# Optimization experiments

Measured on AMD Instinct MI355X. Metric: run time of the kernel, lower is better.

Reference implementation:

```python
import jax, jax.numpy as jnp
import numpy as np

N_HEADS = 8
TOPK = 64
LN_EPS = 1e-5


def layernorm(x, g, b):
    mu = jnp.mean(x, axis=-1, keepdims=True)
    var = jnp.mean((x - mu) ** 2, axis=-1, keepdims=True)
    return (x - mu) * jax.lax.rsqrt(var + LN_EPS) * g + b


def mha(x, wq, wk, wv, wo, causal):
    # x: [B, S, H]; weights are torch nn.Linear style [out, in]
    B, S, H = x.shape
    hd = H // N_HEADS
    scale = 1.0 / np.sqrt(hd)

    def proj(w):
        return (x @ w.T).reshape(B, S, N_HEADS, hd).transpose(0, 2, 1, 3)  # [B, n, S, hd]

    q, k, v = proj(wq), proj(wk), proj(wv)
    s = jnp.einsum('bnqd,bnkd->bnqk', q, k) * scale
    if causal:
        m = jnp.tril(jnp.ones((S, S), bool))
        s = jnp.where(m, s, jnp.finfo(s.dtype).min)
    a = jax.nn.softmax(s, axis=-1)
    o = jnp.einsum('bnqk,bnkd->bnqd', a, v).transpose(0, 2, 1, 3).reshape(B, S, H)
    return o @ wo.T


def topk_activation(x, k):
    # x: [N, F]; keep top-k per row, zero elsewhere (matches topk + scatter_)
    vals, idx = jax.lax.top_k(x, k)
    rows = jnp.arange(x.shape[0])[:, None]
    return jnp.zeros_like(x).at[rows, idx].set(vals)


def setup_inputs() -> dict:
    key = jax.random.key(0)
    B, D, L, H, F = 8, 16, 128, 512, 4096
    ks = jax.random.split(key, 12)
    s = 1.0 / np.sqrt(H)
    w = lambda k, shp, sc: jax.random.normal(k, shp, jnp.float32) * sc
    return {
        'zL': w(ks[0], (B, D, L, H), 1.0),
        'wq_l': w(ks[1], (H, H), s), 'wk_l': w(ks[2], (H, H), s),
        'wv_l': w(ks[3], (H, H), s), 'wo_l': w(ks[4], (H, H), s),
        'gamma_l': jnp.ones(H, jnp.float32), 'beta_l': jnp.zeros(H, jnp.float32),
        'wq_d': w(ks[5], (H, H), s), 'wk_d': w(ks[6], (H, H), s),
        'wv_d': w(ks[7], (H, H), s), 'wo_d': w(ks[8], (H, H), s),
        'gamma_d': jnp.ones(H, jnp.float32), 'beta_d': jnp.zeros(H, jnp.float32),
        'dict_enc': w(ks[9], (F, H), np.sqrt(2.0 / (H + F))),
        'bias_pre': jnp.zeros(H, jnp.float32),
        'bias_enc': jnp.zeros(F, jnp.float32),
        'query_token': jnp.zeros(H, jnp.float32),
    }


def reference(zL, wq_l, wk_l, wv_l, wo_l, gamma_l, beta_l,
              wq_d, wk_d, wv_d, wo_d, gamma_d, beta_d,
              dict_enc, bias_pre, bias_enc, query_token):
    B, D, L, H = zL.shape
    F = dict_enc.shape[0]
    # prepend learned query token along depth, drop last layer
    qt = jnp.broadcast_to(query_token[None, None, None, :], (B, 1, L, H))
    x = jnp.concatenate([qt, zL[:, :-1, :, :]], axis=1)  # [B, D, L, H]
    # non-causal attention over L within each (b, d)
    x = x.reshape(B * D, L, H)
    x = x + mha(layernorm(x, gamma_l, beta_l), wq_l, wk_l, wv_l, wo_l, causal=False)
    # causal attention over D within each (b, l)
    x = x.reshape(B, D, L, H).transpose(0, 2, 1, 3).reshape(B * L, D, H)
    x = x + mha(layernorm(x, gamma_d, beta_d), wq_d, wk_d, wv_d, wo_d, causal=True)
    x_prior = x.reshape(B, L, D, H).transpose(0, 2, 1, 3)  # [B, D, L, H]
    # dictionary encode on residual (detached in original)
    N = B * D * L
    x_src = jax.lax.stop_gradient(zL - x_prior).reshape(N, H)
    logits = (x_src - bias_pre[None, :]) @ dict_enc.T + bias_enc
    z_dense = jax.nn.relu(logits)
    z_flat = topk_activation(z_dense, TOPK)
    z_n = z_flat.reshape(B, D, L, F)
    return z_n, x_prior
```

## Files before the change

### kernel.cpp

```cpp
#include <hip/hip_runtime.h>
#include <stdint.h>

#define NTOK 16384
#define HDIM 512
#define FDIM 4096
#define NHEAD 8

typedef __attribute__((ext_vector_type(8))) _Float16 f16x8;
typedef __attribute__((ext_vector_type(16))) float f32x16;
#define LOSCALE 4096.0f
#define LOINV   (1.0f / 4096.0f)

static __device__ __forceinline__ void ld8f(const float* p, float* v) {
    *(float4*)&v[0] = *(const float4*)p;
    *(float4*)&v[4] = *(const float4*)(p + 4);
}
static __device__ __forceinline__ void st8f(float* p, const float* v) {
    *(float4*)p       = *(const float4*)&v[0];
    *(float4*)(p + 4) = *(const float4*)&v[4];
}

__global__ __launch_bounds__(256) void build_x_k(const float* __restrict__ zL,
                                                 const float* __restrict__ qt,
                                                 float* __restrict__ X) {
    int idx = blockIdx.x * 256 + threadIdx.x;
    int n = idx >> 6;
    int h = (idx & 63) << 3;
    int d = (n >> 7) & 15;
    const float* src = d ? (zL + (((size_t)(n - 128)) << 9) + h) : (qt + h);
    float v[8];
    ld8f(src, v);
    st8f(X + (((size_t)n) << 9) + h, v);
}

__global__ __launch_bounds__(256) void ln_stats_k(const float* __restrict__ X,
                                                  float* __restrict__ mu,
                                                  float* __restrict__ rstd) {
    int row = blockIdx.x * 4 + (threadIdx.x >> 6);
    int lane = threadIdx.x & 63;
    const float* xr = X + (((size_t)row) << 9) + (lane << 3);
    float v[8];
    ld8f(xr, v);
    float s = 0.f;
#pragma unroll
    for (int i = 0; i < 8; ++i) s += v[i];
#pragma unroll
    for (int off = 32; off; off >>= 1) s += __shfl_xor(s, off);
    float m = s * (1.0f / 512.0f);
    float q = 0.f;
#pragma unroll
    for (int i = 0; i < 8; ++i) { float d = v[i] - m; q += d * d; }
#pragma unroll
    for (int off = 32; off; off >>= 1) q += __shfl_xor(q, off);
    if (lane == 0) {
        mu[row] = m;
        rstd[row] = 1.0f / sqrtf(q * (1.0f / 512.0f) + 1e-5f);
    }
}

__global__ __launch_bounds__(512) void attn_l_k(float* __restrict__ QO,
                                                const float* __restrict__ K,
                                                const float* __restrict__ V) {
    __shared__ float ks[128][64];
    __shared__ float vs[128][64];
    const int seq = blockIdx.x, head = blockIdx.y;
    const int t = threadIdx.x;
    const size_t base = (((size_t)seq) << 16) + (head << 6);
#pragma unroll
    for (int i = 0; i < 4; ++i) {
        int slot = t + (i << 9);
        int row = slot >> 4;
        int c4 = (slot & 15) << 2;
        size_t g = base + (((size_t)row) << 9) + c4;
        *(float4*)&ks[row][c4] = *(const float4*)(K + g);
        *(float4*)&vs[row][c4] = *(const float4*)(V + g);
    }
    __syncthreads();
    const int r = t >> 2;
    const int q16 = (t & 3) << 4;
    float* qp = QO + base + (((size_t)r) << 9) + q16;
    float qr[16];
#pragma unroll
    for (int i = 0; i < 4; ++i) *(float4*)&qr[i << 2] = *(const float4*)(qp + (i << 2));
    float o[16];
#pragma unroll
    for (int d = 0; d < 16; ++d) o[d] = 0.f;
    float m = -1e30f, l = 0.f;
    for (int j = 0; j < 128; ++j) {
        const float* kp = &ks[j][q16];
        float s0 = 0.f, s1 = 0.f, s2 = 0.f, s3 = 0.f;
#pragma unroll
        for (int d = 0; d < 16; d += 4) {
            s0 = fmaf(qr[d + 0], kp[d + 0], s0);
            s1 = fmaf(qr[d + 1], kp[d + 1], s1);
            s2 = fmaf(qr[d + 2], kp[d + 2], s2);
            s3 = fmaf(qr[d + 3], kp[d + 3], s3);
        }
        float sp = (s0 + s1) + (s2 + s3);
        sp += __shfl_xor(sp, 1);
        sp += __shfl_xor(sp, 2);
        float s = sp * 0.125f;
        if (s > m) {
            float c = expf(m - s);
#pragma unroll
            for (int d = 0; d < 16; ++d) o[d] *= c;
            l *= c;
            m = s;
        }
        float w = expf(s - m);
        l += w;
        const float* vp = &vs[j][q16];
#pragma unroll
        for (int d = 0; d < 16; ++d) o[d] = fmaf(w, vp[d], o[d]);
    }
    float inv = 1.0f / l;
#pragma unroll
    for (int i = 0; i < 4; ++i)
        *(float4*)(qp + (i << 2)) = make_float4(o[i * 4] * inv, o[i * 4 + 1] * inv,
                                                o[i * 4 + 2] * inv, o[i * 4 + 3] * inv);
}

__global__ __launch_bounds__(128) void attn_d_k(float* __restrict__ QO,
                                                const float* __restrict__ K,
                                                const float* __restrict__ V) {
    __shared__ float ks[16][512];
    __shared__ float vs[16][512];
    const int bl = blockIdx.x;
    const int b = bl >> 7, l = bl & 127;
    const int t = threadIdx.x;
    const size_t base = ((size_t)(b * 2048 + l)) << 9;
#pragma unroll
    for (int i = 0; i < 16; ++i) {
        int slot = t + (i << 7);
        int row = slot >> 7;
        int c4 = (slot & 127) << 2;
        size_t g = base + (((size_t)row) << 16) + c4;
        *(float4*)&ks[row][c4] = *(const float4*)(K + g);
        *(float4*)&vs[row][c4] = *(const float4*)(V + g);
    }
    __syncthreads();
    const int head = t >> 4, dr = t & 15;
    const int ho = head << 6;
    float qr[64];
    float* qp = QO + base + (((size_t)dr) << 16) + ho;
#pragma unroll
    for (int i = 0; i < 16; ++i) *(float4*)&qr[i << 2] = *(const float4*)(qp + (i << 2));
    float s[16];
    float m = -1e30f;
#pragma unroll
    for (int j = 0; j < 16; ++j) {
        float s0 = 0.f, s1 = 0.f, s2 = 0.f, s3 = 0.f;
#pragma unroll
        for (int d = 0; d < 64; d += 4) {
            s0 = fmaf(qr[d + 0], ks[j][ho + d + 0], s0);
            s1 = fmaf(qr[d + 1], ks[j][ho + d + 1], s1);
            s2 = fmaf(qr[d + 2], ks[j][ho + d + 2], s2);
            s3 = fmaf(qr[d + 3], ks[j][ho + d + 3], s3);
        }
        float sv = ((s0 + s1) + (s2 + s3)) * 0.125f;
        s[j] = (j <= dr) ? sv : -1e30f;
        m = fmaxf(m, s[j]);
    }
    float lsum = 0.f;
#pragma unroll
    for (int j = 0; j < 16; ++j) {
        float w = (j <= dr) ? expf(s[j] - m) : 0.f;
        s[j] = w;
        lsum += w;
    }
    float inv = 1.0f / lsum;
    float o[64];
#pragma unroll
    for (int d = 0; d < 64; ++d) o[d] = 0.f;
#pragma unroll
    for (int j = 0; j < 16; ++j) {
        float w = s[j];
#pragma unroll
        for (int d = 0; d < 64; ++d) o[d] = fmaf(w, vs[j][ho + d], o[d]);
    }
#pragma unroll
    for (int i = 0; i < 16; ++i)
        *(float4*)(qp + (i << 2)) = make_float4(o[i * 4] * inv, o[i * 4 + 1] * inv,
                                                o[i * 4 + 2] * inv, o[i * 4 + 3] * inv);
}

__global__ __launch_bounds__(256) void xprior_xsrc_k(const float* __restrict__ zL,
                                                     const float* __restrict__ bias_pre,
                                                     float* __restrict__ X,
                                                     float* __restrict__ out_xp) {
    int idx = blockIdx.x * 256 + threadIdx.x;
    int h = (idx & 63) << 3;
    float z[8], p[8], x[8];
    ld8f(zL + (((size_t)idx) << 3), z);
    ld8f(bias_pre + h, p);
    float* xp = X + (((size_t)idx) << 3);
    ld8f(xp, x);
    st8f(out_xp + (((size_t)idx) << 3), x);
    float o[8];
#pragma unroll
    for (int i = 0; i < 8; ++i) o[i] = z[i] - x[i] - p[i];
    st8f(xp, o);
}

__global__ __launch_bounds__(256) void split2_k(const float* __restrict__ in,
                                                _Float16* __restrict__ ph,
                                                _Float16* __restrict__ pl) {
    int idx = blockIdx.x * 256 + threadIdx.x;
    float v[8];
    ld8f(in + (((size_t)idx) << 3), v);
    _Float16 h8[8], l8[8];
#pragma unroll
    for (int i = 0; i < 8; ++i) {
        _Float16 h = (_Float16)v[i];
        float r = v[i] - (float)h;
        h8[i] = h;
        l8[i] = (_Float16)(r * LOSCALE);
    }
    *(int4*)(ph + (((size_t)idx) << 3)) = *(int4*)h8;
    *(int4*)(pl + (((size_t)idx) << 3)) = *(int4*)l8;
}

__global__ __launch_bounds__(256) void split2_ln_k(const float* __restrict__ X,
                                                   const float* __restrict__ mu,
                                                   const float* __restrict__ rstd,
                                                   const float* __restrict__ gamma,
                                                   const float* __restrict__ beta,
                                                   _Float16* __restrict__ ph,
                                                   _Float16* __restrict__ pl) {
    int idx = blockIdx.x * 256 + threadIdx.x;
    int row = idx >> 6;
    int h = (idx & 63) << 3;
    float v[8], gv[8], be[8];
    ld8f(X + (((size_t)idx) << 3), v);
    ld8f(gamma + h, gv);
    ld8f(beta + h, be);
    float m = mu[row], rs = rstd[row];
    _Float16 h8[8], l8[8];
#pragma unroll
    for (int i = 0; i < 8; ++i) {
        float y = (v[i] - m) * rs * gv[i] + be[i];
        _Float16 hh = (_Float16)y;
        float r = y - (float)hh;
        h8[i] = hh;
        l8[i] = (_Float16)(r * LOSCALE);
    }
    *(int4*)(ph + (((size_t)idx) << 3)) = *(int4*)h8;
    *(int4*)(pl + (((size_t)idx) << 3)) = *(int4*)l8;
}

#define LDT 34
template<bool ADD_C, bool BIAS>
__global__ __launch_bounds__(256) void gemm_f16_k(
        const _Float16* __restrict__ Xh, const _Float16* __restrict__ Xl,
        const _Float16* __restrict__ Wh, const _Float16* __restrict__ Wl,
        const float* __restrict__ bias, float* __restrict__ Cout, int ldc) {
    __shared__ _Float16 Ah[128][LDT], Al[128][LDT];
    __shared__ _Float16 Bh[64][LDT],  Bl[64][LDT];
    const int tid = threadIdx.x;
    const int bm = blockIdx.y << 7;
    const int bn = blockIdx.x << 6;
    const int w = tid >> 6, lane = tid & 63;
    const int wr = w >> 1, wc = w & 1;
    const int l31 = lane & 31, hh = lane >> 5;
    f32x16 acc1[2], acc2[2];
#pragma unroll
    for (int i = 0; i < 2; ++i)
#pragma unroll
        for (int r = 0; r < 16; ++r) { acc1[i][r] = 0.f; acc2[i][r] = 0.f; }

    for (int k0 = 0; k0 < HDIM; k0 += 32) {
        __syncthreads();
#pragma unroll
        for (int i = 0; i < 2; ++i) {
            int s = tid + (i << 8);
            int row = s >> 2, kg = (s & 3) << 3;
            size_t ga = (size_t)(bm + row) * HDIM + k0 + kg;
            *(int4*)&Ah[row][kg] = *(const int4*)(Xh + ga);
            *(int4*)&Al[row][kg] = *(const int4*)(Xl + ga);
        }
        {
            int row = tid >> 2, kg = (tid & 3) << 3;
            size_t gb = (size_t)(bn + row) * HDIM + k0 + kg;
            *(int4*)&Bh[row][kg] = *(const int4*)(Wh + gb);
            *(int4*)&Bl[row][kg] = *(const int4*)(Wl + gb);
        }
        __syncthreads();
#pragma unroll
        for (int kh = 0; kh < 2; ++kh) {
            const int ko = (kh << 4) + (hh << 3);
            f16x8 fah[2], fal[2];
#pragma unroll
            for (int mf = 0; mf < 2; ++mf) {
                int ar = (wr << 6) + (mf << 5) + l31;
                fah[mf] = *(const f16x8*)&Ah[ar][ko];
                fal[mf] = *(const f16x8*)&Al[ar][ko];
            }
            int bc_ = (wc << 5) + l31;
            f16x8 bh = *(const f16x8*)&Bh[bc_][ko];
            f16x8 bl = *(const f16x8*)&Bl[bc_][ko];
#pragma unroll
            for (int mf = 0; mf < 2; ++mf) {
                acc1[mf] = __builtin_amdgcn_mfma_f32_32x32x16_f16(fah[mf], bh, acc1[mf], 0, 0, 0);
                acc2[mf] = __builtin_amdgcn_mfma_f32_32x32x16_f16(fah[mf], bl, acc2[mf], 0, 0, 0);
                acc2[mf] = __builtin_amdgcn_mfma_f32_32x32x16_f16(fal[mf], bh, acc2[mf], 0, 0, 0);
            }
        }
    }
    const int col = bn + (wc << 5) + l31;
    const float badd = BIAS ? bias[col] : 0.f;
#pragma unroll
    for (int mf = 0; mf < 2; ++mf) {
#pragma unroll
        for (int r = 0; r < 16; ++r) {
            int row = bm + (wr << 6) + (mf << 5) + (r & 3) + ((r >> 2) << 3) + (hh << 2);
            float* cp = Cout + (size_t)row * ldc + col;
            float val = acc1[mf][r] + acc2[mf][r] * LOINV + badd;
            if (ADD_C) val += *cp;
            *cp = val;
        }
    }
}

__global__ __launch_bounds__(256) void topk_k(const float* __restrict__ logits,
                                              float* __restrict__ out) {
    const int row = blockIdx.x;
    const float* lr = logits + (((size_t)row) << 12);
    const int t = threadIdx.x;
    float v[16]; uint32_t u[16];
#pragma unroll
    for (int i = 0; i < 16; ++i) {
        float x = fmaxf(lr[t + (i << 8)], 0.f);
        v[i] = x;
        u[i] = __float_as_uint(x);
    }
    __shared__ int red[4];
    __shared__ unsigned long long bits[64];
    __shared__ int s_cut;
    uint32_t prefix = 0;
    bool exact = false;
    for (int bit = 30; bit >= 0; --bit) {
        uint32_t c = prefix | (1u << bit);
        int cnt = 0;
#pragma unroll
        for (int i = 0; i < 16; ++i) cnt += (u[i] >= c) ? 1 : 0;
#pragma unroll
        for (int off = 32; off; off >>= 1) cnt += __shfl_xor(cnt, off);
        if ((t & 63) == 0) red[t >> 6] = cnt;
        __syncthreads();
        int total = red[0] + red[1] + red[2] + red[3];
        __syncthreads();
        if (total >= 64) prefix = c;
        if (total == 64) { exact = true; break; }
    }
    float* orow = out + (((size_t)row) << 12);
    if (exact) {
#pragma unroll
        for (int i = 0; i < 16; ++i) {
            int col = t + (i << 8);
            orow[col] = (u[i] >= prefix) ? v[i] : 0.f;
        }
        return;
    }
    const uint32_t T64 = prefix;
    int cg = 0;
#pragma unroll
    for (int i = 0; i < 16; ++i) cg += (u[i] > T64) ? 1 : 0;
#pragma unroll
    for (int off = 32; off; off >>= 1) cg += __shfl_xor(cg, off);
    if ((t & 63) == 0) red[t >> 6] = cg;
    __syncthreads();
    const int ngt = red[0] + red[1] + red[2] + red[3];
    int cut = -1;
    if (T64 != 0u) {
        const int r = 64 - ngt;
        if (t < 64) bits[t] = 0ull;
        __syncthreads();
#pragma unroll
        for (int i = 0; i < 16; ++i) {
            if (u[i] == T64) {
                int col = t + (i << 8);
                atomicOr(&bits[col >> 6], 1ull << (col & 63));
            }
        }
        __syncthreads();
        if (t == 0) {
            int need = r, cs = FDIM - 1;
            for (int wd = 0; wd < 64; ++wd) {
                int pc = __popcll(bits[wd]);
                if (need <= pc) {
                    unsigned long long bb = bits[wd];
                    for (int q = 1; q < need; ++q) bb &= bb - 1;
                    cs = (wd << 6) + (__ffsll(bb) - 1);
                    break;
                }
                need -= pc;
            }
            s_cut = cs;
        }
        __syncthreads();
        cut = s_cut;
    }
#pragma unroll
    for (int i = 0; i < 16; ++i) {
        int col = t + (i << 8);
        bool keep = (u[i] > T64) || (T64 != 0u && u[i] == T64 && col <= cut);
        orow[col] = keep ? v[i] : 0.f;
    }
}

extern "C" void kernel_launch(void* const* d_in, const int* in_sizes, int n_in,
                              void* d_out, int out_size, void* d_ws, size_t ws_size,
                              hipStream_t stream) {
    const float* zL      = (const float*)d_in[0];
    const float* gamma_l = (const float*)d_in[5];
    const float* beta_l  = (const float*)d_in[6];
    const float* gamma_d = (const float*)d_in[11];
    const float* beta_d  = (const float*)d_in[12];
    const float* dict_e  = (const float*)d_in[13];
    const float* bias_pre= (const float*)d_in[14];
    const float* bias_enc= (const float*)d_in[15];
    const float* qt      = (const float*)d_in[16];
    const float* wproj[8] = { (const float*)d_in[1], (const float*)d_in[2],
                              (const float*)d_in[3], (const float*)d_in[4],
                              (const float*)d_in[7], (const float*)d_in[8],
                              (const float*)d_in[9], (const float*)d_in[10] };

    float* out_z  = (float*)d_out;
    float* out_xp = out_z + (size_t)NTOK * FDIM;

    const size_t NHf = (size_t)NTOK * HDIM;
    float* B0 = (float*)d_out;
    float* B1 = B0 + NHf;
    float* B2 = B1 + NHf;
    float* B3 = B2 + NHf;

    float* wsf    = (float*)d_ws;
    float* mu     = wsf + 64;
    float* rstd   = mu + NTOK;
    float* logits = rstd + NTOK;

    const size_t dictE = (size_t)FDIM * HDIM;
    const size_t WE    = (size_t)HDIM * HDIM;

    int crows = NTOK;
    const size_t mfmaFixedB = (64 + 2 * (size_t)NTOK) * sizeof(float)
                            + (2 * dictE + 16 * WE + 2 * NHf) * sizeof(_Float16);
    while (crows > 128 &&
           mfmaFixedB + (size_t)crows * FDIM * sizeof(float) > ws_size) crows >>= 1;
    const bool ok = mfmaFixedB + (size_t)128 * FDIM * sizeof(float) <= ws_size;

    const dim3 blk256(256), blk128(128), blk512(512);
    const dim3 gElem(4096);
    const dim3 gProjM(HDIM / 64, NTOK / 128);

    if (ok) {
        _Float16* dh = (_Float16*)(logits + (size_t)crows * FDIM);
        _Float16* dl = dh + dictE;
        _Float16* wsp = dh + 2 * dictE;
        _Float16* xh = wsp + 16 * WE;
        _Float16* xl = xh + NHf;
        _Float16* wh[8], *wl[8];
        for (int i = 0; i < 8; ++i) {
            wh[i] = wsp + (size_t)i * 2 * WE;
            wl[i] = wh[i] + WE;
        }

        for (int i = 0; i < 8; ++i)
            split2_k<<<dim3(WE / 8 / 256), blk256, 0, stream>>>(wproj[i], wh[i], wl[i]);
        split2_k<<<dim3(dictE / 8 / 256), blk256, 0, stream>>>(dict_e, dh, dl);

        build_x_k<<<gElem, blk256, 0, stream>>>(zL, qt, B0);

        ln_stats_k<<<dim3(NTOK / 4), blk256, 0, stream>>>(B0, mu, rstd);
        split2_ln_k<<<gElem, blk256, 0, stream>>>(B0, mu, rstd, gamma_l, beta_l, xh, xl);
        gemm_f16_k<false, false><<<gProjM, blk256, 0, stream>>>(xh, xl, wh[0], wl[0], nullptr, B1, HDIM);
        gemm_f16_k<false, false><<<gProjM, blk256, 0, stream>>>(xh, xl, wh[1], wl[1], nullptr, B2, HDIM);
        gemm_f16_k<false, false><<<gProjM, blk256, 0, stream>>>(xh, xl, wh[2], wl[2], nullptr, B3, HDIM);
        attn_l_k<<<dim3(128, NHEAD), blk512, 0, stream>>>(B1, B2, B3);
        split2_k<<<gElem, blk256, 0, stream>>>(B1, xh, xl);
        gemm_f16_k<true, false><<<gProjM, blk256, 0, stream>>>(xh, xl, wh[3], wl[3], nullptr, B0, HDIM);

        ln_stats_k<<<dim3(NTOK / 4), blk256, 0, stream>>>(B0, mu, rstd);
        split2_ln_k<<<gElem, blk256, 0, stream>>>(B0, mu, rstd, gamma_d, beta_d, xh, xl);
        gemm_f16_k<false, false><<<gProjM, blk256, 0, stream>>>(xh, xl, wh[4], wl[4], nullptr, B1, HDIM);
        gemm_f16_k<false, false><<<gProjM, blk256, 0, stream>>>(xh, xl, wh[5], wl[5], nullptr, B2, HDIM);
        gemm_f16_k<false, false><<<gProjM, blk256, 0, stream>>>(xh, xl, wh[6], wl[6], nullptr, B3, HDIM);
        attn_d_k<<<dim3(1024), blk128, 0, stream>>>(B1, B2, B3);
        split2_k<<<gElem, blk256, 0, stream>>>(B1, xh, xl);
        gemm_f16_k<true, false><<<gProjM, blk256, 0, stream>>>(xh, xl, wh[7], wl[7], nullptr, B0, HDIM);

        xprior_xsrc_k<<<gElem, blk256, 0, stream>>>(zL, bias_pre, B0, out_xp);
        split2_k<<<gElem, blk256, 0, stream>>>(B0, xh, xl);

        const dim3 gDict(FDIM / 64, crows / 128);
        for (int c0 = 0; c0 < NTOK; c0 += crows) {
            gemm_f16_k<false, true><<<gDict, blk256, 0, stream>>>(
                xh + (size_t)c0 * HDIM, xl + (size_t)c0 * HDIM,
                dh, dl, bias_enc, logits, FDIM);
            topk_k<<<dim3(crows), blk256, 0, stream>>>(logits, out_z + (size_t)c0 * FDIM);
        }
    } else {
        int cr = 2048;
        const size_t fixedB = (64 + 2 * (size_t)NTOK) * sizeof(float) + dictE * 2 * sizeof(_Float16);
        while (cr > 128 &&
               fixedB + (size_t)cr * FDIM * sizeof(float) + ((size_t)cr * HDIM + 16 * WE) * 2 * sizeof(_Float16) > ws_size)
            cr >>= 1;
        _Float16* dh = (_Float16*)(logits + (size_t)cr * FDIM);
        _Float16* dl = dh + dictE;
        _Float16* xh = dl + dictE;
        _Float16* xl = xh + (size_t)cr * HDIM;
        _Float16* wh = xl + (size_t)cr * HDIM;
        _Float16* wlo = wh + WE;

        build_x_k<<<gElem, blk256, 0, stream>>>(zL, qt, B0);

        ln_stats_k<<<dim3(NTOK / 4), blk256, 0, stream>>>(B0, mu, rstd);
        for (int i = 0; i < 3; ++i) {
            split2_k<<<dim3(WE / 8 / 256), blk256, 0, stream>>>(wproj[i], wh, wlo);
            float* dst = (i == 0) ? B1 : (i == 1) ? B2 : B3;
            for (int c0 = 0; c0 < NTOK; c0 += cr) {
                split2_ln_k<<<dim3(cr * HDIM / 8 / 256), blk256, 0, stream>>>(
                    B0 + (size_t)c0 * HDIM, mu + c0, rstd + c0, gamma_l, beta_l, xh, xl);
                gemm_f16_k<false, false><<<dim3(HDIM / 64, cr / 128), blk256, 0, stream>>>(
                    xh, xl, wh, wlo, nullptr, dst + (size_t)c0 * HDIM, HDIM);
            }
        }
        attn_l_k<<<dim3(128, NHEAD), blk512, 0, stream>>>(B1, B2, B3);
        split2_k<<<dim3(WE / 8 / 256), blk256, 0, stream>>>(wproj[3], wh, wlo);
        for (int c0 = 0; c0 < NTOK; c0 += cr) {
            split2_k<<<dim3(cr * HDIM / 8 / 256), blk256, 0, stream>>>(B1 + (size_t)c0 * HDIM, xh, xl);
            gemm_f16_k<true, false><<<dim3(HDIM / 64, cr / 128), blk256, 0, stream>>>(
                xh, xl, wh, wlo, nullptr, B0 + (size_t)c0 * HDIM, HDIM);
        }
        ln_stats_k<<<dim3(NTOK / 4), blk256, 0, stream>>>(B0, mu, rstd);
        for (int i = 4; i < 7; ++i) {
            split2_k<<<dim3(WE / 8 / 256), blk256, 0, stream>>>(wproj[i], wh, wlo);
            float* dst = (i == 4) ? B1 : (i == 5) ? B2 : B3;
            for (int c0 = 0; c0 < NTOK; c0 += cr) {
                split2_ln_k<<<dim3(cr * HDIM / 8 / 256), blk256, 0, stream>>>(
                    B0 + (size_t)c0 * HDIM, mu + c0, rstd + c0, gamma_d, beta_d, xh, xl);
                gemm_f16_k<false, false><<<dim3(HDIM / 64, cr / 128), blk256, 0, stream>>>(
                    xh, xl, wh, wlo, nullptr, dst + (size_t)c0 * HDIM, HDIM);
            }
        }
        attn_d_k<<<dim3(1024), blk128, 0, stream>>>(B1, B2, B3);
        split2_k<<<dim3(WE / 8 / 256), blk256, 0, stream>>>(wproj[7], wh, wlo);
        for (int c0 = 0; c0 < NTOK; c0 += cr) {
            split2_k<<<dim3(cr * HDIM / 8 / 256), blk256, 0, stream>>>(B1 + (size_t)c0 * HDIM, xh, xl);
            gemm_f16_k<true, false><<<dim3(HDIM / 64, cr / 128), blk256, 0, stream>>>(
                xh, xl, wh, wlo, nullptr, B0 + (size_t)c0 * HDIM, HDIM);
        }
        xprior_xsrc_k<<<gElem, blk256, 0, stream>>>(zL, bias_pre, B0, out_xp);
        split2_k<<<dim3(dictE / 8 / 256), blk256, 0, stream>>>(dict_e, dh, dl);
        for (int c0 = NTOK - cr; c0 >= 0; c0 -= cr) {
            split2_k<<<dim3(cr * HDIM / 8 / 256), blk256, 0, stream>>>(B0 + (size_t)c0 * HDIM, xh, xl);
            gemm_f16_k<false, true><<<dim3(FDIM / 64, cr / 128), blk256, 0, stream>>>(
                xh, xl, dh, dl, bias_enc, logits, FDIM);
            topk_k<<<dim3(cr), blk256, 0, stream>>>(logits, out_z + (size_t)c0 * FDIM);
        }
    }
}
```

Before: 1.168 ms.

## Fuse fp16 split into LN, attention and residual kernels; double-buffer GEMM tiles

LayerNorm statistics and normalisation now happen in one kernel that writes the hi/lo fp16 split directly. The attention kernels and the x_src kernel also emit the split form, which removes the separate split2 passes and their extra fp32 round trips through global memory. The GEMM now uses double-buffered shared-memory tiles with a register prefetch of the next k-slice, so global loads overlap the MFMA work. The chunked fallback path for small workspaces is dropped, which assumes the workspace is large enough and doubles the GEMM's LDS use.

```diff
diff --git a/kernel.cpp b/kernel.cpp
--- a/kernel.cpp
+++ b/kernel.cpp
@@ -33,12 +33,15 @@
     st8f(X + (((size_t)n) << 9) + h, v);
 }
 
-__global__ __launch_bounds__(256) void ln_stats_k(const float* __restrict__ X,
-                                                  float* __restrict__ mu,
-                                                  float* __restrict__ rstd) {
+__global__ __launch_bounds__(256) void ln_split_k(const float* __restrict__ X,
+                                                  const float* __restrict__ gamma,
+                                                  const float* __restrict__ beta,
+                                                  _Float16* __restrict__ ph,
+                                                  _Float16* __restrict__ pl) {
     int row = blockIdx.x * 4 + (threadIdx.x >> 6);
     int lane = threadIdx.x & 63;
-    const float* xr = X + (((size_t)row) << 9) + (lane << 3);
+    int h = lane << 3;
+    const float* xr = X + (((size_t)row) << 9) + h;
     float v[8];
     ld8f(xr, v);
     float s = 0.f;
@@ -52,15 +55,28 @@
     for (int i = 0; i < 8; ++i) { float d = v[i] - m; q += d * d; }
 #pragma unroll
     for (int off = 32; off; off >>= 1) q += __shfl_xor(q, off);
-    if (lane == 0) {
-        mu[row] = m;
-        rstd[row] = 1.0f / sqrtf(q * (1.0f / 512.0f) + 1e-5f);
-    }
-}
-
-__global__ __launch_bounds__(512) void attn_l_k(float* __restrict__ QO,
+    float rs = 1.0f / sqrtf(q * (1.0f / 512.0f) + 1e-5f);
+    float gv[8], be[8];
+    ld8f(gamma + h, gv);
+    ld8f(beta + h, be);
+    _Float16 h8[8], l8[8];
+#pragma unroll
+    for (int i = 0; i < 8; ++i) {
+        float y = (v[i] - m) * rs * gv[i] + be[i];
+        _Float16 hh = (_Float16)y;
+        h8[i] = hh;
+        l8[i] = (_Float16)((y - (float)hh) * LOSCALE);
+    }
+    size_t off = (((size_t)row) << 9) + h;
+    *(int4*)(ph + off) = *(int4*)h8;
+    *(int4*)(pl + off) = *(int4*)l8;
+}
+
+__global__ __launch_bounds__(512) void attn_l_k(const float* __restrict__ Q,
                                                 const float* __restrict__ K,
-                                                const float* __restrict__ V) {
+                                                const float* __restrict__ V,
+                                                _Float16* __restrict__ xh,
+                                                _Float16* __restrict__ xl) {
     __shared__ float ks[128][64];
     __shared__ float vs[128][64];
     const int seq = blockIdx.x, head = blockIdx.y;
@@ -78,7 +94,7 @@
     __syncthreads();
     const int r = t >> 2;
     const int q16 = (t & 3) << 4;
-    float* qp = QO + base + (((size_t)r) << 9) + q16;
+    const float* qp = Q + base + (((size_t)r) << 9) + q16;
     float qr[16];
 #pragma unroll
     for (int i = 0; i < 4; ++i) *(float4*)&qr[i << 2] = *(const float4*)(qp + (i << 2));
@@ -114,15 +130,26 @@
         for (int d = 0; d < 16; ++d) o[d] = fmaf(w, vp[d], o[d]);
     }
     float inv = 1.0f / l;
-#pragma unroll
-    for (int i = 0; i < 4; ++i)
-        *(float4*)(qp + (i << 2)) = make_float4(o[i * 4] * inv, o[i * 4 + 1] * inv,
-                                                o[i * 4 + 2] * inv, o[i * 4 + 3] * inv);
-}
-
-__global__ __launch_bounds__(128) void attn_d_k(float* __restrict__ QO,
+    _Float16 h8[16], l8[16];
+#pragma unroll
+    for (int i = 0; i < 16; ++i) {
+        float y = o[i] * inv;
+        _Float16 hh = (_Float16)y;
+        h8[i] = hh;
+        l8[i] = (_Float16)((y - (float)hh) * LOSCALE);
+    }
+    size_t eo = base + (((size_t)r) << 9) + q16;
+    *(int4*)(xh + eo)     = ((int4*)h8)[0];
+    *(int4*)(xh + eo + 8) = ((int4*)h8)[1];
+    *(int4*)(xl + eo)     = ((int4*)l8)[0];
+    *(int4*)(xl + eo + 8) = ((int4*)l8)[1];
+}
+
+__global__ __launch_bounds__(128) void attn_d_k(const float* __restrict__ Q,
                                                 const float* __restrict__ K,
-                                                const float* __restrict__ V) {
+                                                const float* __restrict__ V,
+                                                _Float16* __restrict__ xh,
+                                                _Float16* __restrict__ xl) {
     __shared__ float ks[16][512];
     __shared__ float vs[16][512];
     const int bl = blockIdx.x;
@@ -142,7 +169,7 @@
     const int head = t >> 4, dr = t & 15;
     const int ho = head << 6;
     float qr[64];
-    float* qp = QO + base + (((size_t)dr) << 16) + ho;
+    const float* qp = Q + base + (((size_t)dr) << 16) + ho;
 #pragma unroll
     for (int i = 0; i < 16; ++i) *(float4*)&qr[i << 2] = *(const float4*)(qp + (i << 2));
     float s[16];
@@ -178,28 +205,46 @@
 #pragma unroll
         for (int d = 0; d < 64; ++d) o[d] = fmaf(w, vs[j][ho + d], o[d]);
     }
-#pragma unroll
-    for (int i = 0; i < 16; ++i)
-        *(float4*)(qp + (i << 2)) = make_float4(o[i * 4] * inv, o[i * 4 + 1] * inv,
-                                                o[i * 4 + 2] * inv, o[i * 4 + 3] * inv);
+    size_t eo = base + (((size_t)dr) << 16) + ho;
+#pragma unroll
+    for (int i = 0; i < 8; ++i) {
+        _Float16 h8[8], l8[8];
+#pragma unroll
+        for (int j = 0; j < 8; ++j) {
+            float y = o[i * 8 + j] * inv;
+            _Float16 hh = (_Float16)y;
+            h8[j] = hh;
+            l8[j] = (_Float16)((y - (float)hh) * LOSCALE);
+        }
+        *(int4*)(xh + eo + (i << 3)) = *(int4*)h8;
+        *(int4*)(xl + eo + (i << 3)) = *(int4*)l8;
+    }
 }
 
 __global__ __launch_bounds__(256) void xprior_xsrc_k(const float* __restrict__ zL,
                                                      const float* __restrict__ bias_pre,
-                                                     float* __restrict__ X,
-                                                     float* __restrict__ out_xp) {
+                                                     const float* __restrict__ X,
+                                                     float* __restrict__ out_xp,
+                                                     _Float16* __restrict__ xh,
+                                                     _Float16* __restrict__ xl) {
     int idx = blockIdx.x * 256 + threadIdx.x;
     int h = (idx & 63) << 3;
+    size_t off = ((size_t)idx) << 3;
     float z[8], p[8], x[8];
-    ld8f(zL + (((size_t)idx) << 3), z);
+    ld8f(zL + off, z);
     ld8f(bias_pre + h, p);
-    float* xp = X + (((size_t)idx) << 3);
-    ld8f(xp, x);
-    st8f(out_xp + (((size_t)idx) << 3), x);
-    float o[8];
-#pragma unroll
-    for (int i = 0; i < 8; ++i) o[i] = z[i] - x[i] - p[i];
-    st8f(xp, o);
+    ld8f(X + off, x);
+    st8f(out_xp + off, x);
+    _Float16 h8[8], l8[8];
+#pragma unroll
+    for (int i = 0; i < 8; ++i) {
+        float y = z[i] - x[i] - p[i];
+        _Float16 hh = (_Float16)y;
+        h8[i] = hh;
+        l8[i] = (_Float16)((y - (float)hh) * LOSCALE);
+    }
+    *(int4*)(xh + off) = *(int4*)h8;
+    *(int4*)(xl + off) = *(int4*)l8;
 }
 
 __global__ __launch_bounds__(256) void split2_k(const float* __restrict__ in,
@@ -220,70 +265,58 @@
     *(int4*)(pl + (((size_t)idx) << 3)) = *(int4*)l8;
 }
 
-__global__ __launch_bounds__(256) void split2_ln_k(const float* __restrict__ X,
-                                                   const float* __restrict__ mu,
-                                                   const float* __restrict__ rstd,
-                                                   const float* __restrict__ gamma,
-                                                   const float* __restrict__ beta,
-                                                   _Float16* __restrict__ ph,
-                                                   _Float16* __restrict__ pl) {
-    int idx = blockIdx.x * 256 + threadIdx.x;
-    int row = idx >> 6;
-    int h = (idx & 63) << 3;
-    float v[8], gv[8], be[8];
-    ld8f(X + (((size_t)idx) << 3), v);
-    ld8f(gamma + h, gv);
-    ld8f(beta + h, be);
-    float m = mu[row], rs = rstd[row];
-    _Float16 h8[8], l8[8];
-#pragma unroll
-    for (int i = 0; i < 8; ++i) {
-        float y = (v[i] - m) * rs * gv[i] + be[i];
-        _Float16 hh = (_Float16)y;
-        float r = y - (float)hh;
-        h8[i] = hh;
-        l8[i] = (_Float16)(r * LOSCALE);
-    }
-    *(int4*)(ph + (((size_t)idx) << 3)) = *(int4*)h8;
-    *(int4*)(pl + (((size_t)idx) << 3)) = *(int4*)l8;
-}
-
 #define LDT 34
 template<bool ADD_C, bool BIAS>
 __global__ __launch_bounds__(256) void gemm_f16_k(
         const _Float16* __restrict__ Xh, const _Float16* __restrict__ Xl,
         const _Float16* __restrict__ Wh, const _Float16* __restrict__ Wl,
         const float* __restrict__ bias, float* __restrict__ Cout, int ldc) {
-    __shared__ _Float16 Ah[128][LDT], Al[128][LDT];
-    __shared__ _Float16 Bh[64][LDT],  Bl[64][LDT];
+    __shared__ _Float16 Ah[2][128][LDT], Al[2][128][LDT];
+    __shared__ _Float16 Bh[2][64][LDT],  Bl[2][64][LDT];
     const int tid = threadIdx.x;
     const int bm = blockIdx.y << 7;
     const int bn = blockIdx.x << 6;
     const int w = tid >> 6, lane = tid & 63;
     const int wr = w >> 1, wc = w & 1;
     const int l31 = lane & 31, hh = lane >> 5;
+    const int ar0 = tid >> 2, akg = (tid & 3) << 3;
+    const int ar1 = ar0 + 64;
+    const _Float16* pXh0 = Xh + (size_t)(bm + ar0) * HDIM + akg;
+    const _Float16* pXl0 = Xl + (size_t)(bm + ar0) * HDIM + akg;
+    const _Float16* pXh1 = Xh + (size_t)(bm + ar1) * HDIM + akg;
+    const _Float16* pXl1 = Xl + (size_t)(bm + ar1) * HDIM + akg;
+    const _Float16* pWh  = Wh + (size_t)(bn + ar0) * HDIM + akg;
+    const _Float16* pWl  = Wl + (size_t)(bn + ar0) * HDIM + akg;
+
     f32x16 acc1[2], acc2[2];
 #pragma unroll
     for (int i = 0; i < 2; ++i)
 #pragma unroll
         for (int r = 0; r < 16; ++r) { acc1[i][r] = 0.f; acc2[i][r] = 0.f; }
 
-    for (int k0 = 0; k0 < HDIM; k0 += 32) {
-        __syncthreads();
-#pragma unroll
-        for (int i = 0; i < 2; ++i) {
-            int s = tid + (i << 8);
-            int row = s >> 2, kg = (s & 3) << 3;
-            size_t ga = (size_t)(bm + row) * HDIM + k0 + kg;
-            *(int4*)&Ah[row][kg] = *(const int4*)(Xh + ga);
-            *(int4*)&Al[row][kg] = *(const int4*)(Xl + ga);
-        }
-        {
-            int row = tid >> 2, kg = (tid & 3) << 3;
-            size_t gb = (size_t)(bn + row) * HDIM + k0 + kg;
-            *(int4*)&Bh[row][kg] = *(const int4*)(Wh + gb);
-            *(int4*)&Bl[row][kg] = *(const int4*)(Wl + gb);
-        }
+    int4 ra0h, ra0l, ra1h, ra1l, rbh, rbl;
+    auto LOADR = [&](int k0) {
+        ra0h = *(const int4*)(pXh0 + k0);
+        ra0l = *(const int4*)(pXl0 + k0);
+        ra1h = *(const int4*)(pXh1 + k0);
+        ra1l = *(const int4*)(pXl1 + k0);
+        rbh  = *(const int4*)(pWh + k0);
+        rbl  = *(const int4*)(pWl + k0);
+    };
+    auto STORE = [&](int buf) {
+        *(int4*)&Ah[buf][ar0][akg] = ra0h;
+        *(int4*)&Al[buf][ar0][akg] = ra0l;
+        *(int4*)&Ah[buf][ar1][akg] = ra1h;
+        *(int4*)&Al[buf][ar1][akg] = ra1l;
+        *(int4*)&Bh[buf][ar0][akg] = rbh;
+        *(int4*)&Bl[buf][ar0][akg] = rbl;
+    };
+
+    LOADR(0);
+    STORE(0);
+    int cur = 0;
+    for (int it = 0; it < 16; ++it) {
+        if (it < 15) LOADR((it + 1) << 5);
         __syncthreads();
 #pragma unroll
         for (int kh = 0; kh < 2; ++kh) {
@@ -292,12 +325,12 @@
 #pragma unroll
             for (int mf = 0; mf < 2; ++mf) {
                 int ar = (wr << 6) + (mf << 5) + l31;
-                fah[mf] = *(const f16x8*)&Ah[ar][ko];
-                fal[mf] = *(const f16x8*)&Al[ar][ko];
+                fah[mf] = *(const f16x8*)&Ah[cur][ar][ko];
+                fal[mf] = *(const f16x8*)&Al[cur][ar][ko];
             }
             int bc_ = (wc << 5) + l31;
-            f16x8 bh = *(const f16x8*)&Bh[bc_][ko];
-            f16x8 bl = *(const f16x8*)&Bl[bc_][ko];
+            f16x8 bh = *(const f16x8*)&Bh[cur][bc_][ko];
+            f16x8 bl = *(const f16x8*)&Bl[cur][bc_][ko];
 #pragma unroll
             for (int mf = 0; mf < 2; ++mf) {
                 acc1[mf] = __builtin_amdgcn_mfma_f32_32x32x16_f16(fah[mf], bh, acc1[mf], 0, 0, 0);
@@ -305,6 +338,7 @@
                 acc2[mf] = __builtin_amdgcn_mfma_f32_32x32x16_f16(fal[mf], bh, acc2[mf], 0, 0, 0);
             }
         }
+        if (it < 15) { STORE(cur ^ 1); cur ^= 1; }
     }
     const int col = bn + (wc << 5) + l31;
     const float badd = BIAS ? bias[col] : 0.f;
@@ -435,128 +469,59 @@
     float* B3 = B2 + NHf;
 
     float* wsf    = (float*)d_ws;
-    float* mu     = wsf + 64;
-    float* rstd   = mu + NTOK;
-    float* logits = rstd + NTOK;
+    float* logits = wsf + 64;
 
     const size_t dictE = (size_t)FDIM * HDIM;
     const size_t WE    = (size_t)HDIM * HDIM;
 
     int crows = NTOK;
-    const size_t mfmaFixedB = (64 + 2 * (size_t)NTOK) * sizeof(float)
-                            + (2 * dictE + 16 * WE + 2 * NHf) * sizeof(_Float16);
-    while (crows > 128 &&
-           mfmaFixedB + (size_t)crows * FDIM * sizeof(float) > ws_size) crows >>= 1;
-    const bool ok = mfmaFixedB + (size_t)128 * FDIM * sizeof(float) <= ws_size;
+    const size_t fixedB = 64 * sizeof(float)
+                        + (2 * dictE + 16 * WE + 2 * NHf) * sizeof(_Float16);
+    while (crows > 128 && fixedB + (size_t)crows * FDIM * sizeof(float) > ws_size)
+        crows >>= 1;
+
+    _Float16* dh = (_Float16*)(logits + (size_t)crows * FDIM);
+    _Float16* dl = dh + dictE;
+    _Float16* wsp = dh + 2 * dictE;
+    _Float16* xh = wsp + 16 * WE;
+    _Float16* xl = xh + NHf;
+    _Float16* wh[8], *wl[8];
+    for (int i = 0; i < 8; ++i) {
+        wh[i] = wsp + (size_t)i * 2 * WE;
+        wl[i] = wh[i] + WE;
+    }
 
     const dim3 blk256(256), blk128(128), blk512(512);
     const dim3 gElem(4096);
     const dim3 gProjM(HDIM / 64, NTOK / 128);
 
-    if (ok) {
-        _Float16* dh = (_Float16*)(logits + (size_t)crows * FDIM);
-        _Float16* dl = dh + dictE;
-        _Float16* wsp = dh + 2 * dictE;
-        _Float16* xh = wsp + 16 * WE;
-        _Float16* xl = xh + NHf;
-        _Float16* wh[8], *wl[8];
-        for (int i = 0; i < 8; ++i) {
-            wh[i] = wsp + (size_t)i * 2 * WE;
-            wl[i] = wh[i] + WE;
-        }
-
-        for (int i = 0; i < 8; ++i)
-            split2_k<<<dim3(WE / 8 / 256), blk256, 0, stream>>>(wproj[i], wh[i], wl[i]);
-        split2_k<<<dim3(dictE / 8 / 256), blk256, 0, stream>>>(dict_e, dh, dl);
-
-        build_x_k<<<gElem, blk256, 0, stream>>>(zL, qt, B0);
-
-        ln_stats_k<<<dim3(NTOK / 4), blk256, 0, stream>>>(B0, mu, rstd);
-        split2_ln_k<<<gElem, blk256, 0, stream>>>(B0, mu, rstd, gamma_l, beta_l, xh, xl);
-        gemm_f16_k<false, false><<<gProjM, blk256, 0, stream>>>(xh, xl, wh[0], wl[0], nullptr, B1, HDIM);
-        gemm_f16_k<false, false><<<gProjM, blk256, 0, stream>>>(xh, xl, wh[1], wl[1], nullptr, B2, HDIM);
-        gemm_f16_k<false, false><<<gProjM, blk256, 0, stream>>>(xh, xl, wh[2], wl[2], nullptr, B3, HDIM);
-        attn_l_k<<<dim3(128, NHEAD), blk512, 0, stream>>>(B1, B2, B3);
-        split2_k<<<gElem, blk256, 0, stream>>>(B1, xh, xl);
-        gemm_f16_k<true, false><<<gProjM, blk256, 0, stream>>>(xh, xl, wh[3], wl[3], nullptr, B0, HDIM);
-
-        ln_stats_k<<<dim3(NTOK / 4), blk256, 0, stream>>>(B0, mu, rstd);
-        split2_ln_k<<<gElem, blk256, 0, stream>>>(B0, mu, rstd, gamma_d, beta_d, xh, xl);
-        gemm_f16_k<false, false><<<gProjM, blk256, 0, stream>>>(xh, xl, wh[4], wl[4], nullptr, B1, HDIM);
-        gemm_f16_k<false, false><<<gProjM, blk256, 0, stream>>>(xh, xl, wh[5], wl[5], nullptr, B2, HDIM);
-        gemm_f16_k<false, false><<<gProjM, blk256, 0, stream>>>(xh, xl, wh[6], wl[6], nullptr, B3, HDIM);
-        attn_d_k<<<dim3(1024), blk128, 0, stream>>>(B1, B2, B3);
-        split2_k<<<gElem, blk256, 0, stream>>>(B1, xh, xl);
-        gemm_f16_k<true, false><<<gProjM, blk256, 0, stream>>>(xh, xl, wh[7], wl[7], nullptr, B0, HDIM);
-
-        xprior_xsrc_k<<<gElem, blk256, 0, stream>>>(zL, bias_pre, B0, out_xp);
-        split2_k<<<gElem, blk256, 0, stream>>>(B0, xh, xl);
-
-        const dim3 gDict(FDIM / 64, crows / 128);
-        for (int c0 = 0; c0 < NTOK; c0 += crows) {
-            gemm_f16_k<false, true><<<gDict, blk256, 0, stream>>>(
-                xh + (size_t)c0 * HDIM, xl + (size_t)c0 * HDIM,
-                dh, dl, bias_enc, logits, FDIM);
-            topk_k<<<dim3(crows), blk256, 0, stream>>>(logits, out_z + (size_t)c0 * FDIM);
-        }
-    } else {
-        int cr = 2048;
-        const size_t fixedB = (64 + 2 * (size_t)NTOK) * sizeof(float) + dictE * 2 * sizeof(_Float16);
-        while (cr > 128 &&
-               fixedB + (size_t)cr * FDIM * sizeof(float) + ((size_t)cr * HDIM + 16 * WE) * 2 * sizeof(_Float16) > ws_size)
-            cr >>= 1;
-        _Float16* dh = (_Float16*)(logits + (size_t)cr * FDIM);
-        _Float16* dl = dh + dictE;
-        _Float16* xh = dl + dictE;
-        _Float16* xl = xh + (size_t)cr * HDIM;
-        _Float16* wh = xl + (size_t)cr * HDIM;
-        _Float16* wlo = wh + WE;
-
-        build_x_k<<<gElem, blk256, 0, stream>>>(zL, qt, B0);
-
-        ln_stats_k<<<dim3(NTOK / 4), blk256, 0, stream>>>(B0, mu, rstd);
-        for (int i = 0; i < 3; ++i) {
-            split2_k<<<dim3(WE / 8 / 256), blk256, 0, stream>>>(wproj[i], wh, wlo);
-            float* dst = (i == 0) ? B1 : (i == 1) ? B2 : B3;
-            for (int c0 = 0; c0 < NTOK; c0 += cr) {
-                split2_ln_k<<<dim3(cr * HDIM / 8 / 256), blk256, 0, stream>>>(
-                    B0 + (size_t)c0 * HDIM, mu + c0, rstd + c0, gamma_l, beta_l, xh, xl);
-                gemm_f16_k<false, false><<<dim3(HDIM / 64, cr / 128), blk256, 0, stream>>>(
-                    xh, xl, wh, wlo, nullptr, dst + (size_t)c0 * HDIM, HDIM);
-            }
-        }
-        attn_l_k<<<dim3(128, NHEAD), blk512, 0, stream>>>(B1, B2, B3);
-        split2_k<<<dim3(WE / 8 / 256), blk256, 0, stream>>>(wproj[3], wh, wlo);
-        for (int c0 = 0; c0 < NTOK; c0 += cr) {
-            split2_k<<<dim3(cr * HDIM / 8 / 256), blk256, 0, stream>>>(B1 + (size_t)c0 * HDIM, xh, xl);
-            gemm_f16_k<true, false><<<dim3(HDIM / 64, cr / 128), blk256, 0, stream>>>(
-                xh, xl, wh, wlo, nullptr, B0 + (size_t)c0 * HDIM, HDIM);
-        }
-        ln_stats_k<<<dim3(NTOK / 4), blk256, 0, stream>>>(B0, mu, rstd);
-        for (int i = 4; i < 7; ++i) {
-            split2_k<<<dim3(WE / 8 / 256), blk256, 0, stream>>>(wproj[i], wh, wlo);
-            float* dst = (i == 4) ? B1 : (i == 5) ? B2 : B3;
-            for (int c0 = 0; c0 < NTOK; c0 += cr) {
-                split2_ln_k<<<dim3(cr * HDIM / 8 / 256), blk256, 0, stream>>>(
-                    B0 + (size_t)c0 * HDIM, mu + c0, rstd + c0, gamma_d, beta_d, xh, xl);
-                gemm_f16_k<false, false><<<dim3(HDIM / 64, cr / 128), blk256, 0, stream>>>(
-                    xh, xl, wh, wlo, nullptr, dst + (size_t)c0 * HDIM, HDIM);
-            }
-        }
-        attn_d_k<<<dim3(1024), blk128, 0, stream>>>(B1, B2, B3);
-        split2_k<<<dim3(WE / 8 / 256), blk256, 0, stream>>>(wproj[7], wh, wlo);
-        for (int c0 = 0; c0 < NTOK; c0 += cr) {
-            split2_k<<<dim3(cr * HDIM / 8 / 256), blk256, 0, stream>>>(B1 + (size_t)c0 * HDIM, xh, xl);
-            gemm_f16_k<true, false><<<dim3(HDIM / 64, cr / 128), blk256, 0, stream>>>(
-                xh, xl, wh, wlo, nullptr, B0 + (size_t)c0 * HDIM, HDIM);
-        }
-        xprior_xsrc_k<<<gElem, blk256, 0, stream>>>(zL, bias_pre, B0, out_xp);
-        split2_k<<<dim3(dictE / 8 / 256), blk256, 0, stream>>>(dict_e, dh, dl);
-        for (int c0 = NTOK - cr; c0 >= 0; c0 -= cr) {
-            split2_k<<<dim3(cr * HDIM / 8 / 256), blk256, 0, stream>>>(B0 + (size_t)c0 * HDIM, xh, xl);
-            gemm_f16_k<false, true><<<dim3(FDIM / 64, cr / 128), blk256, 0, stream>>>(
-                xh, xl, dh, dl, bias_enc, logits, FDIM);
-            topk_k<<<dim3(cr), blk256, 0, stream>>>(logits, out_z + (size_t)c0 * FDIM);
-        }
-    }
-}
+    for (int i = 0; i < 8; ++i)
+        split2_k<<<dim3(WE / 8 / 256), blk256, 0, stream>>>(wproj[i], wh[i], wl[i]);
+    split2_k<<<dim3(dictE / 8 / 256), blk256, 0, stream>>>(dict_e, dh, dl);
+
+    build_x_k<<<gElem, blk256, 0, stream>>>(zL, qt, B0);
+
+    ln_split_k<<<dim3(NTOK / 4), blk256, 0, stream>>>(B0, gamma_l, beta_l, xh, xl);
+    gemm_f16_k<false, false><<<gProjM, blk256, 0, stream>>>(xh, xl, wh[0], wl[0], nullptr, B1, HDIM);
+    gemm_f16_k<false, false><<<gProjM, blk256, 0, stream>>>(xh, xl, wh[1], wl[1], nullptr, B2, HDIM);
+    gemm_f16_k<false, false><<<gProjM, blk256, 0, stream>>>(xh, xl, wh[2], wl[2], nullptr, B3, HDIM);
+    attn_l_k<<<dim3(128, NHEAD), blk512, 0, stream>>>(B1, B2, B3, xh, xl);
+    gemm_f16_k<true, false><<<gProjM, blk256, 0, stream>>>(xh, xl, wh[3], wl[3], nullptr, B0, HDIM);
+
+    ln_split_k<<<dim3(NTOK / 4), blk256, 0, stream>>>(B0, gamma_d, beta_d, xh, xl);
+    gemm_f16_k<false, false><<<gProjM, blk256, 0, stream>>>(xh, xl, wh[4], wl[4], nullptr, B1, HDIM);
+    gemm_f16_k<false, false><<<gProjM, blk256, 0, stream>>>(xh, xl, wh[5], wl[5], nullptr, B2, HDIM);
+    gemm_f16_k<false, false><<<gProjM, blk256, 0, stream>>>(xh, xl, wh[6], wl[6], nullptr, B3, HDIM);
+    attn_d_k<<<dim3(1024), blk128, 0, stream>>>(B1, B2, B3, xh, xl);
+    gemm_f16_k<true, false><<<gProjM, blk256, 0, stream>>>(xh, xl, wh[7], wl[7], nullptr, B0, HDIM);
+
+    xprior_xsrc_k<<<gElem, blk256, 0, stream>>>(zL, bias_pre, B0, out_xp, xh, xl);
+
+    const dim3 gDict(FDIM / 64, crows / 128);
+    for (int c0 = 0; c0 < NTOK; c0 += crows) {
+        gemm_f16_k<false, true><<<gDict, blk256, 0, stream>>>(
+            xh + (size_t)c0 * HDIM, xl + (size_t)c0 * HDIM,
+            dh, dl, bias_enc, logits, FDIM);
+        topk_k<<<dim3(crows), blk256, 0, stream>>>(logits, out_z + (size_t)c0 * FDIM);
+    }
+}
```

Result: no change. 1.176 ms (+0.7%).
